# Performance work log

Measured on AMD Instinct MI355X. Metric: run time of the kernel, lower is better.

Reference implementation:

```python
import jax, jax.numpy as jnp
import numpy as np

B, C, H, W = 64, 3, 512, 512
MIN = 0.33  # min crop fraction from __init__


def setup_inputs() -> dict:
    key = jax.random.key(0)
    k1, k2, k3, k4, k5 = jax.random.split(key, 5)
    img = jax.random.normal(k1, (B, C, H, W), jnp.float32)
    # Replicate the module's internal randint sampling for the crop boxes.
    min_h, min_w = int(MIN * H), int(MIN * W)
    hight = jax.random.randint(k2, (B,), min_h, H)
    width = jax.random.randint(k3, (B,), min_w, W)
    yc = jax.random.randint(k4, (B,), min_h // 2, H)
    xc = jax.random.randint(k5, (B,), min_w // 2, W)
    y1 = jnp.clip(yc - hight // 2, 0, H).astype(jnp.int32)
    y2 = jnp.clip(yc + hight // 2, 0, H).astype(jnp.int32)
    x1 = jnp.clip(xc - width // 2, 0, W).astype(jnp.int32)
    x2 = jnp.clip(xc + width // 2, 0, W).astype(jnp.int32)
    return {"img": img, "y1": y1, "y2": y2, "x1": x1, "x2": x2}


def _axis_coords(start, end, out_size):
    # Source coords for bilinear resize, align_corners=False (torch default).
    n = (end - start).astype(jnp.float32)  # crop length along this axis
    s = (jnp.arange(out_size, dtype=jnp.float32) + 0.5) * n / out_size - 0.5
    s = jnp.clip(s, 0.0, n - 1.0)
    i0 = jnp.floor(s).astype(jnp.int32)
    i1 = jnp.minimum(i0 + 1, end - start - 1)
    wgt = s - i0.astype(jnp.float32)
    return start + i0, start + i1, wgt  # absolute indices into the full image


def _resize_one(img_b, y1, y2, x1, x2):
    # img_b: [C, H, W]; crop [y1:y2, x1:x2] then bilinear-resize back to (H, W)
    iy0, iy1, wy = _axis_coords(y1, y2, H)
    ix0, ix1, wx = _axis_coords(x1, x2, W)
    r0 = jnp.take(img_b, iy0, axis=1)
    r1 = jnp.take(img_b, iy1, axis=1)
    rows = r0 + (r1 - r0) * wy[None, :, None]      # [C, H, W] rows interpolated
    c0 = jnp.take(rows, ix0, axis=2)
    c1 = jnp.take(rows, ix1, axis=2)
    return c0 + (c1 - c0) * wx[None, None, :]      # [C, H, W]


def reference(img, y1, y2, x1, x2):
    return jax.vmap(_resize_one)(img, y1, y2, x1, x2)
```

## Files before the change

kernel.cpp:

```cpp
#include <hip/hip_runtime.h>


#define BB 64
#define CC 3
#define HH 512
#define WW 512
#define NB (BB * HH)
#define PITCH 516

typedef const __attribute__((address_space(1))) void g_void;
typedef __attribute__((address_space(3))) void l_void;

__global__ __launch_bounds__(256) void rand_crop_resize_kernel(
    const float* __restrict__ img,
    const int* __restrict__ y1a, const int* __restrict__ y2a,
    const int* __restrict__ x1a, const int* __restrict__ x2a,
    float* __restrict__ out)
{
    __shared__ float s[6 * PITCH];

    const int r  = (blockIdx.x & 7) * (NB / 8) + (blockIdx.x >> 3);
    const int oy = r & (HH - 1);
    const int b  = r >> 9;

    const int Y1 = y1a[b], Y2 = y2a[b], X1 = x1a[b], X2 = x2a[b];

    const int ny_i = Y2 - Y1;
    float sy = ((float)oy + 0.5f) * (float)ny_i * (1.0f / 512.0f) - 0.5f;
    sy = fminf(fmaxf(sy, 0.0f), (float)ny_i - 1.0f);
    int iy0 = (int)sy;
    const int iy1 = min(iy0 + 1, ny_i - 1) + Y1;
    const float wy = sy - (float)iy0;
    iy0 += Y1;

    const int t = threadIdx.x;

    const int nx_i = X2 - X1;
    const int c0   = X1 >> 2;
    const int c1   = min((X1 + nx_i) >> 2, (WW >> 2) - 1);
    const int nch  = c1 - c0 + 1;
    const int xoff = X1 - (c0 << 2);
    const int zi   = xoff + nx_i;

    if (t < 6) s[t * PITCH + zi] = 0.0f;

    const size_t base = (size_t)b * (size_t)(CC * HH * WW);
    const int g  = t >> 7;
    const int tt = t & 127;
    if (tt < nch) {
        #pragma unroll
        for (int k = 0; k < 3; ++k) {
            const int rw = 3 * g + k;
            const int c  = rw >> 1;
            const int iy = (rw & 1) ? iy1 : iy0;
            const float* gsrc = img + base
                + (size_t)(c * HH + iy) * (size_t)WW + (size_t)((c0 + tt) << 2);
            float* ldst = s + rw * PITCH + (tt << 2);
            __builtin_amdgcn_global_load_lds((g_void*)gsrc, (l_void*)ldst,
                                             16, 0, 0);
        }
    }
    __syncthreads();

    const float nx    = (float)nx_i;
    const float nxm1f = nx - 1.0f;

    float2 res[3];
    #pragma unroll
    for (int k = 0; k < 2; ++k) {
        const int ox = 2 * t + k;
        float sx = ((float)ox + 0.5f) * nx * (1.0f / 512.0f) - 0.5f;
        sx = fminf(fmaxf(sx, 0.0f), nxm1f);
        const int   ix0 = (int)sx;
        const float wx  = sx - (float)ix0;
        const int   ix  = xoff + ix0;

        #pragma unroll
        for (int c = 0; c < 3; ++c) {
            const float* s0 = s + (2 * c) * PITCH;
            const float* s1 = s0 + PITCH;
            const float v00 = s0[ix];
            const float v01 = s0[ix + 1];
            const float v10 = s1[ix];
            const float v11 = s1[ix + 1];
            const float r0v = v00 + (v10 - v00) * wy;
            const float r1v = v01 + (v11 - v01) * wy;
            const float v   = r0v + (r1v - r0v) * wx;
            if (k == 0) res[c].x = v; else res[c].y = v;
        }
    }

    #pragma unroll
    for (int c = 0; c < 3; ++c) {
        float2* orow = (float2*)(out
            + ((size_t)(b * CC + c) * (size_t)HH + (size_t)oy) * (size_t)WW);
        orow[t] = res[c];
    }
}

extern "C" void kernel_launch(void* const* d_in, const int* in_sizes, int n_in,
                              void* d_out, int out_size, void* d_ws, size_t ws_size,
                              hipStream_t stream) {
    const float* img = (const float*)d_in[0];
    const int*   y1  = (const int*)d_in[1];
    const int*   y2  = (const int*)d_in[2];
    const int*   x1  = (const int*)d_in[3];
    const int*   x2  = (const int*)d_in[4];
    float*       out = (float*)d_out;

    dim3 grid(NB);
    dim3 block(256);
    hipLaunchKernelGGL(rand_crop_resize_kernel, grid, block, 0, stream,
                       img, y1, y2, x1, x2, out);
}
```

Before: 323.8 us.

## Process four output rows per block, sharing staged source rows in LDS

Each block now computes four consecutive output rows instead of one. It loads the contiguous span of source rows they need (up to five per channel) into LDS once, and the load work is spread across the four waves. This cuts redundant global reads of shared source rows and reduces the block count and per-block overhead, in exchange for more LDS per block and a longer serial loop per thread.

```diff
diff --git a/kernel.cpp b/kernel.cpp
--- a/kernel.cpp
+++ b/kernel.cpp
@@ -6,6 +6,9 @@
 #define HH 512
 #define WW 512
 #define NB (BB * HH)
+#define TILES 4
+#define NBAND (NB / TILES)
+#define NR 5
 #define PITCH 516
 
 typedef const __attribute__((address_space(1))) void g_void;
@@ -17,23 +20,31 @@
     const int* __restrict__ x1a, const int* __restrict__ x2a,
     float* __restrict__ out)
 {
-    __shared__ float s[6 * PITCH];
+    __shared__ float s[3 * NR * PITCH];
 
-    const int r  = (blockIdx.x & 7) * (NB / 8) + (blockIdx.x >> 3);
-    const int oy = r & (HH - 1);
-    const int b  = r >> 9;
+    const int j   = (blockIdx.x & 7) * (NBAND / 8) + (blockIdx.x >> 3);
+    const int r0  = j * TILES;
+    const int b   = r0 >> 9;
+    const int oy0 = r0 & (HH - 1);
 
     const int Y1 = y1a[b], Y2 = y2a[b], X1 = x1a[b], X2 = x2a[b];
-
-    const int ny_i = Y2 - Y1;
-    float sy = ((float)oy + 0.5f) * (float)ny_i * (1.0f / 512.0f) - 0.5f;
-    sy = fminf(fmaxf(sy, 0.0f), (float)ny_i - 1.0f);
-    int iy0 = (int)sy;
-    const int iy1 = min(iy0 + 1, ny_i - 1) + Y1;
-    const float wy = sy - (float)iy0;
-    iy0 += Y1;
+    const int   ny_i = Y2 - Y1;
+    const float nyf  = (float)ny_i;
 
     const int t = threadIdx.x;
+
+    int iy0q[TILES], iy1q[TILES]; float wyq[TILES];
+    #pragma unroll
+    for (int q = 0; q < TILES; ++q) {
+        float syv = ((float)(oy0 + q) + 0.5f) * nyf * (1.0f / 512.0f) - 0.5f;
+        syv = fminf(fmaxf(syv, 0.0f), nyf - 1.0f);
+        const int i0 = (int)syv;
+        wyq[q]  = syv - (float)i0;
+        iy1q[q] = min(i0 + 1, ny_i - 1) + Y1;
+        iy0q[q] = i0 + Y1;
+    }
+    const int rlo   = iy0q[0];
+    const int nrows = iy1q[TILES - 1] - rlo + 1;
 
     const int nx_i = X2 - X1;
     const int c0   = X1 >> 2;
@@ -42,59 +53,81 @@
     const int xoff = X1 - (c0 << 2);
     const int zi   = xoff + nx_i;
 
-    if (t < 6) s[t * PITCH + zi] = 0.0f;
+    if (t < 3 * NR) s[t * PITCH + zi] = 0.0f;
 
     const size_t base = (size_t)b * (size_t)(CC * HH * WW);
-    const int g  = t >> 7;
-    const int tt = t & 127;
-    if (tt < nch) {
+    const int wave = t >> 6;
+    const int lane = t & 63;
+    #pragma unroll
+    for (int c = 0; c < 3; ++c) {
         #pragma unroll
-        for (int k = 0; k < 3; ++k) {
-            const int rw = 3 * g + k;
-            const int c  = rw >> 1;
-            const int iy = (rw & 1) ? iy1 : iy0;
-            const float* gsrc = img + base
-                + (size_t)(c * HH + iy) * (size_t)WW + (size_t)((c0 + tt) << 2);
-            float* ldst = s + rw * PITCH + (tt << 2);
-            __builtin_amdgcn_global_load_lds((g_void*)gsrc, (l_void*)ldst,
-                                             16, 0, 0);
+        for (int rr = 0; rr < NR; ++rr) {
+            #pragma unroll
+            for (int h = 0; h < 2; ++h) {
+                const int idx = (c * NR + rr) * 2 + h;
+                if (((idx & 3) == wave) && rr < nrows) {
+                    const int ch = h * 64 + lane;
+                    if (ch < nch) {
+                        const int iy = rlo + rr;
+                        const float* gsrc = img + base
+                            + (size_t)(c * HH + iy) * (size_t)WW
+                            + (size_t)((c0 + ch) << 2);
+                        float* ldst = s + (c * NR + rr) * PITCH + (ch << 2);
+                        __builtin_amdgcn_global_load_lds((g_void*)gsrc,
+                                                         (l_void*)ldst,
+                                                         16, 0, 0);
+                    }
+                }
+            }
         }
     }
     __syncthreads();
 
-    const float nx    = (float)nx_i;
-    const float nxm1f = nx - 1.0f;
-
-    float2 res[3];
+    const float nx = (float)nx_i, nxm1f = nx - 1.0f;
+    int ixk[2]; float wxk[2];
     #pragma unroll
     for (int k = 0; k < 2; ++k) {
         const int ox = 2 * t + k;
         float sx = ((float)ox + 0.5f) * nx * (1.0f / 512.0f) - 0.5f;
         sx = fminf(fmaxf(sx, 0.0f), nxm1f);
-        const int   ix0 = (int)sx;
-        const float wx  = sx - (float)ix0;
-        const int   ix  = xoff + ix0;
+        const int ix0 = (int)sx;
+        wxk[k] = sx - (float)ix0;
+        ixk[k] = xoff + ix0;
+    }
+
+    #pragma unroll
+    for (int q = 0; q < TILES; ++q) {
+        const int   r0q = iy0q[q] - rlo;
+        const int   r1q = iy1q[q] - rlo;
+        const float wy  = wyq[q];
+
+        float2 res[3];
+        #pragma unroll
+        for (int k = 0; k < 2; ++k) {
+            const int   ix = ixk[k];
+            const float wx = wxk[k];
+            #pragma unroll
+            for (int c = 0; c < 3; ++c) {
+                const float* s0 = s + (c * NR + r0q) * PITCH;
+                const float* s1 = s + (c * NR + r1q) * PITCH;
+                const float v00 = s0[ix];
+                const float v01 = s0[ix + 1];
+                const float v10 = s1[ix];
+                const float v11 = s1[ix + 1];
+                const float r0v = v00 + (v10 - v00) * wy;
+                const float r1v = v01 + (v11 - v01) * wy;
+                const float v   = r0v + (r1v - r0v) * wx;
+                if (k == 0) res[c].x = v; else res[c].y = v;
+            }
+        }
 
         #pragma unroll
         for (int c = 0; c < 3; ++c) {
-            const float* s0 = s + (2 * c) * PITCH;
-            const float* s1 = s0 + PITCH;
-            const float v00 = s0[ix];
-            const float v01 = s0[ix + 1];
-            const float v10 = s1[ix];
-            const float v11 = s1[ix + 1];
-            const float r0v = v00 + (v10 - v00) * wy;
-            const float r1v = v01 + (v11 - v01) * wy;
-            const float v   = r0v + (r1v - r0v) * wx;
-            if (k == 0) res[c].x = v; else res[c].y = v;
+            float2* orow = (float2*)(out
+                + ((size_t)(b * CC + c) * (size_t)HH + (size_t)(oy0 + q))
+                  * (size_t)WW);
+            orow[t] = res[c];
         }
-    }
-
-    #pragma unroll
-    for (int c = 0; c < 3; ++c) {
-        float2* orow = (float2*)(out
-            + ((size_t)(b * CC + c) * (size_t)HH + (size_t)oy) * (size_t)WW);
-        orow[t] = res[c];
     }
 }
 
@@ -108,7 +141,7 @@
     const int*   x2  = (const int*)d_in[4];
     float*       out = (float*)d_out;
 
-    dim3 grid(NB);
+    dim3 grid(NBAND);
     dim3 block(256);
     hipLaunchKernelGGL(rand_crop_resize_kernel, grid, block, 0, stream,
                        img, y1, y2, x1, x2, out);
```

Result: faster. 317.3 us (-2.0%).
